# Kernel optimization log

Hardware: AMD Instinct MI355X
Metric: run time of the kernel (lower is better)

Reference implementation:

```python
import jax, jax.numpy as jnp
import numpy as np

B, S, DIN = 4, 2048, 1024
H, D = 16, 64  # num_head, per-head dim_out


def _xavier(key, shape):
    fan_in, fan_out = shape[0], shape[1]
    limit = float(np.sqrt(6.0 / (fan_in + fan_out)))
    return jax.random.uniform(key, shape, jnp.float32, -limit, limit)


def setup_inputs() -> dict:
    key = jax.random.key(0)
    k_x, k_q, k_k, k_v, k_o = jax.random.split(key, 5)
    inputs = jax.random.normal(k_x, (B, S, DIN), jnp.float32)
    # weights stored as [in, out] (transpose of torch Linear.weight); bias zeros
    return {
        "inputs": inputs,
        "wq": _xavier(k_q, (DIN, H * D)), "bq": jnp.zeros((H * D,), jnp.float32),
        "wk": _xavier(k_k, (DIN, H * D)), "bk": jnp.zeros((H * D,), jnp.float32),
        "wv": _xavier(k_v, (DIN, H * D)), "bv": jnp.zeros((H * D,), jnp.float32),
        "wo": _xavier(k_o, (H * D, D)),  "bo": jnp.zeros((D,), jnp.float32),
    }


def reference(inputs, wq, bq, wk, bk, wv, bv, wo, bo):
    b, s, _ = inputs.shape
    q = (inputs @ wq + bq).reshape(b, s, H, D).transpose(0, 2, 1, 3)  # bhsd
    k = (inputs @ wk + bk).reshape(b, s, H, D).transpose(0, 2, 1, 3)
    v = (inputs @ wv + bv).reshape(b, s, H, D).transpose(0, 2, 1, 3)
    scores = jnp.einsum('bhsd,bhSd->bhsS', q, k) / jnp.sqrt(jnp.float32(D))
    p = jax.nn.softmax(scores, axis=-1)
    o = jnp.einsum('bhsS,bhSd->bhsd', p, v)
    o = o.transpose(0, 2, 1, 3).reshape(b, s, H * D)
    return o @ wo + bo  # [b, s, D]
```

## Files before the change

kernel.cpp:

```cpp
#include <hip/hip_runtime.h>

typedef __attribute__((ext_vector_type(8))) __bf16 bf16x8;
typedef __attribute__((ext_vector_type(4))) float f32x4;

#define NB   4
#define NS   2048
#define NDIN 1024
#define NH   16
#define ND   64
#define NHD  1024
#define NM   (NB * NS)

__device__ __forceinline__ float bf2f(unsigned short u) {
    unsigned int x = ((unsigned int)u) << 16;
    return __builtin_bit_cast(float, x);
}
__device__ __forceinline__ unsigned short f2bf(float f) {
    unsigned int u = __builtin_bit_cast(unsigned int, f);
    u += 0x7fff + ((u >> 16) & 1);
    return (unsigned short)(u >> 16);
}
__device__ __forceinline__ unsigned int cvt_pk_bf16(float lo, float hi) {
    unsigned int r;
    asm("v_cvt_pk_bf16_f32 %0, %1, %2" : "=v"(r) : "v"(lo), "v"(hi));
    return r;
}
__device__ __forceinline__ void gload16(const unsigned short* g, unsigned short* l) {
    __builtin_amdgcn_global_load_lds((const __attribute__((address_space(1))) unsigned int*)g,
                                     (__attribute__((address_space(3))) unsigned int*)l, 16, 0, 0);
}

__global__ __launch_bounds__(256) void cvt_x(const float* __restrict__ src,
                                             unsigned short* __restrict__ dst) {
    int i = blockIdx.x * 256 + threadIdx.x;
    float4 a = ((const float4*)src)[i * 2];
    float4 b = ((const float4*)src)[i * 2 + 1];
    union { uint4 u; unsigned short s[8]; } o;
    o.s[0] = f2bf(a.x); o.s[1] = f2bf(a.y); o.s[2] = f2bf(a.z); o.s[3] = f2bf(a.w);
    o.s[4] = f2bf(b.x); o.s[5] = f2bf(b.y); o.s[6] = f2bf(b.z); o.s[7] = f2bf(b.w);
    *(uint4*)(dst + (size_t)i * 8) = o.u;
}

__global__ void transpose_cvt3(const float* __restrict__ wq, const float* __restrict__ wk,
                               const float* __restrict__ wv, unsigned short* __restrict__ dst_all) {
    __shared__ unsigned short t[32][33];
    const float* src = blockIdx.z == 0 ? wq : blockIdx.z == 1 ? wk : wv;
    unsigned short* dst = dst_all + (size_t)blockIdx.z * 1024 * 1024;
    int k0 = blockIdx.x * 32, n0 = blockIdx.y * 32;
    int tx = threadIdx.x, ty = threadIdx.y;
#pragma unroll
    for (int i = 0; i < 32; i += 8)
        t[ty + i][tx] = f2bf(src[(size_t)(k0 + ty + i) * 1024 + (n0 + tx)]);
    __syncthreads();
#pragma unroll
    for (int i = 0; i < 32; i += 8)
        dst[(size_t)(n0 + ty + i) * 1024 + (k0 + tx)] = t[tx][ty + i];
}

__global__ void transpose_cvt(const float* __restrict__ src,
                              unsigned short* __restrict__ dst, int K, int N) {
    __shared__ unsigned short t[32][33];
    int k0 = blockIdx.x * 32, n0 = blockIdx.y * 32;
    int tx = threadIdx.x, ty = threadIdx.y;
#pragma unroll
    for (int i = 0; i < 32; i += 8)
        t[ty + i][tx] = f2bf(src[(size_t)(k0 + ty + i) * N + (n0 + tx)]);
    __syncthreads();
#pragma unroll
    for (int i = 0; i < 32; i += 8)
        dst[(size_t)(n0 + ty + i) * K + (k0 + tx)] = t[tx][ty + i];
}

__global__ __launch_bounds__(256) void gemm_qkv(
    const unsigned short* __restrict__ X, const unsigned short* __restrict__ Wt,
    const float* __restrict__ bq, const float* __restrict__ bk,
    const float* __restrict__ bv,
    unsigned short* __restrict__ Q, unsigned short* __restrict__ K,
    unsigned short* __restrict__ V) {
    __shared__ unsigned short Al[128][32];
    __shared__ unsigned short Bl[128][32];
    __shared__ unsigned short Cl[128][128];
    int mb = blockIdx.x * 128;
    int nb = blockIdx.y * 128;
    int tid = threadIdx.x;
    int wid = tid >> 6, lane = tid & 63, quad = lane >> 4, l16 = lane & 15;
    int wm = (wid & 1) * 64, wn = (wid >> 1) * 64;

    int srow = 16 * wid + (lane >> 2);
    int scol = (lane & 3) * 8;
    const unsigned short* pa0 = X + (size_t)(mb + srow) * NDIN + scol;
    const unsigned short* pa1 = pa0 + (size_t)64 * NDIN;
    const unsigned short* pb0 = Wt + (size_t)(nb + srow) * NDIN + scol;
    const unsigned short* pb1 = pb0 + (size_t)64 * NDIN;
    unsigned short* la = &Al[0][0] + wid * 512;
    unsigned short* lb = &Bl[0][0] + wid * 512;

    f32x4 acc[4][4];
#pragma unroll
    for (int i = 0; i < 4; i++)
#pragma unroll
        for (int j = 0; j < 4; j++) acc[i][j] = (f32x4){0.f, 0.f, 0.f, 0.f};

    for (int k0 = 0; k0 < NDIN; k0 += 32) {
        gload16(pa0, la);
        gload16(pa1, la + 2048);
        gload16(pb0, lb);
        gload16(pb1, lb + 2048);
        pa0 += 32; pa1 += 32; pb0 += 32; pb1 += 32;
        __syncthreads();
        bf16x8 af[4], bfr[4];
#pragma unroll
        for (int i = 0; i < 4; i++)
            af[i] = *(const bf16x8*)(&Al[wm + i * 16 + l16][quad * 8]);
#pragma unroll
        for (int j = 0; j < 4; j++)
            bfr[j] = *(const bf16x8*)(&Bl[wn + j * 16 + l16][quad * 8]);
#pragma unroll
        for (int i = 0; i < 4; i++)
#pragma unroll
            for (int j = 0; j < 4; j++)
                acc[i][j] = __builtin_amdgcn_mfma_f32_16x16x32_bf16(af[i], bfr[j], acc[i][j], 0, 0, 0);
        __syncthreads();
    }

    int wsel = nb >> 10;
    const float* bias = (wsel == 0) ? bq : (wsel == 1) ? bk : bv;
    unsigned short* dstp = (wsel == 0) ? Q : (wsel == 1) ? K : V;
#pragma unroll
    for (int i = 0; i < 4; i++)
#pragma unroll
        for (int j = 0; j < 4; j++) {
            int nl = wn + j * 16 + l16;
            float bias_v = bias[(nb & 1023) + nl];
#pragma unroll
            for (int r = 0; r < 4; r++) {
                int ml = wm + i * 16 + quad * 4 + r;
                int pc = ((nl >> 3) ^ (ml & 15));
                Cl[ml][(pc << 3) | (nl & 7)] = f2bf(acc[i][j][r] + bias_v);
            }
        }
    __syncthreads();
    {
        int hl = tid >> 7, sl = tid & 127;
        int h = ((nb & 1023) >> 6) + hl;
        int m = mb + sl, b = m >> 11, sidx = m & 2047;
        unsigned short* orow = dstp + ((size_t)((b * NH + h) * NS + sidx)) * ND;
#pragma unroll
        for (int c = 0; c < 8; c++) {
            int pc = ((hl * 8 + c) ^ (sl & 15));
            *(uint4*)(orow + c * 8) = *(const uint4*)(&Cl[sl][pc << 3]);
        }
    }
}

__global__ __launch_bounds__(256) void attn(
    const unsigned short* __restrict__ Q, const unsigned short* __restrict__ K,
    const unsigned short* __restrict__ V, unsigned short* __restrict__ Obuf) {
    __shared__ unsigned short Kl[2][64][64];
    __shared__ unsigned short Vt[2][64][64];

    int lin = blockIdx.x;
    int xcd = lin & 7, idx = lin >> 3;
    int bh = ((idx >> 4) << 3) | xcd;
    int qt = idx & 15;

    size_t base = (size_t)bh * NS * ND;
    int tid = threadIdx.x, wid = tid >> 6, lane = tid & 63;
    int quad = lane >> 4, l16 = lane & 15;
    int lx = l16 & 7;
    int q0 = qt * 128 + wid * 32;

    bf16x8 qa[2][2];
#pragma unroll
    for (int s = 0; s < 2; s++)
#pragma unroll
        for (int f = 0; f < 2; f++) {
            union { uint4 u; unsigned short sv[8]; } in_, out_;
            in_.u = *(const uint4*)(Q + base + (size_t)(q0 + s * 16 + l16) * ND + f * 32 + quad * 8);
#pragma unroll
            for (int j = 0; j < 8; j++) out_.sv[j] = f2bf(bf2f(in_.sv[j]) * 0.125f);
            qa[s][f] = __builtin_bit_cast(bf16x8, out_.u);
        }

    float lrow[2] = {0.f, 0.f};
    f32x4 o[2][4];
#pragma unroll
    for (int s = 0; s < 2; s++)
#pragma unroll
        for (int t = 0; t < 4; t++) o[s][t] = (f32x4){0.f, 0.f, 0.f, 0.f};

    int c0 = tid, c1 = tid + 256;
    int kr0w = c0 >> 3, kc0 = c0 & 7, kg0c = kc0 ^ (kr0w & 7);
    int kr1w = c1 >> 3, kc1 = c1 & 7, kg1c = kc1 ^ (kr1w & 7);
    const unsigned short* kp0 = K + base + (size_t)kr0w * ND + kc0 * 8;
    const unsigned short* kp1 = K + base + (size_t)kr1w * ND + kc1 * 8;
    int p = tid & 31, dqA = tid >> 5, dqB = dqA + 8;
    int cp = ((p >> 4) << 2) | ((p >> 1) & 3);
    int ps = (((p >> 3) & 1) << 2) | ((p & 1) << 1);
    int cb = cp ^ ((dqA & 1) << 2);
    const unsigned short* vg = V + base + (size_t)(2 * p) * ND + dqA * 4;

    uint4 k0r, k1r;
    uint2 va0, va1, va2, va3;

    auto writeKV = [&](int buf) {
        *(uint4*)(&Kl[buf][kr0w][kg0c * 8]) = k0r;
        *(uint4*)(&Kl[buf][kr1w][kg1c * 8]) = k1r;
        unsigned short* vt = &Vt[buf][0][0];
        unsigned int w0 = __builtin_amdgcn_perm(va1.x, va0.x, 0x05040100u);
        unsigned int w1 = __builtin_amdgcn_perm(va1.x, va0.x, 0x07060302u);
        unsigned int w2 = __builtin_amdgcn_perm(va1.y, va0.y, 0x05040100u);
        unsigned int w3 = __builtin_amdgcn_perm(va1.y, va0.y, 0x07060302u);
        *(unsigned int*)(vt + (dqA * 4 + 0) * 64 + ((cb ^ 0) << 3) + ps) = w0;
        *(unsigned int*)(vt + (dqA * 4 + 1) * 64 + ((cb ^ 1) << 3) + ps) = w1;
        *(unsigned int*)(vt + (dqA * 4 + 2) * 64 + ((cb ^ 2) << 3) + ps) = w2;
        *(unsigned int*)(vt + (dqA * 4 + 3) * 64 + ((cb ^ 3) << 3) + ps) = w3;
        unsigned int x0 = __builtin_amdgcn_perm(va3.x, va2.x, 0x05040100u);
        unsigned int x1 = __builtin_amdgcn_perm(va3.x, va2.x, 0x07060302u);
        unsigned int x2 = __builtin_amdgcn_perm(va3.y, va2.y, 0x05040100u);
        unsigned int x3 = __builtin_amdgcn_perm(va3.y, va2.y, 0x07060302u);
        *(unsigned int*)(vt + (dqB * 4 + 0) * 64 + ((cb ^ 0) << 3) + ps) = x0;
        *(unsigned int*)(vt + (dqB * 4 + 1) * 64 + ((cb ^ 1) << 3) + ps) = x1;
        *(unsigned int*)(vt + (dqB * 4 + 2) * 64 + ((cb ^ 2) << 3) + ps) = x2;
        *(unsigned int*)(vt + (dqB * 4 + 3) * 64 + ((cb ^ 3) << 3) + ps) = x3;
    };

    k0r = *(const uint4*)kp0;
    k1r = *(const uint4*)kp1;
    va0 = *(const uint2*)(vg);
    va1 = *(const uint2*)(vg + ND);
    va2 = *(const uint2*)(vg + 32);
    va3 = *(const uint2*)(vg + ND + 32);
    writeKV(0);
    __syncthreads();

    int cur = 0;
    for (int kc = 0; kc < NS; kc += 64) {
        bool more = (kc + 64 < NS);
        if (more) {
            kp0 += 64 * ND; kp1 += 64 * ND; vg += 64 * ND;
            k0r = *(const uint4*)kp0;
            k1r = *(const uint4*)kp1;
            va0 = *(const uint2*)(vg);
            va1 = *(const uint2*)(vg + ND);
            va2 = *(const uint2*)(vg + 32);
            va3 = *(const uint2*)(vg + ND + 32);
        }

        const unsigned short (*Kc)[64] = Kl[cur];
        const unsigned short (*Vc)[64] = Vt[cur];

        f32x4 st[2][4];
        __builtin_amdgcn_s_setprio(1);
#pragma unroll
        for (int sub = 0; sub < 4; sub++) {
            bf16x8 kb0 = *(const bf16x8*)(&Kc[sub * 16 + l16][((quad ^ lx) << 3)]);
            bf16x8 kb1 = *(const bf16x8*)(&Kc[sub * 16 + l16][(((4 + quad) ^ lx) << 3)]);
#pragma unroll
            for (int s = 0; s < 2; s++) {
                f32x4 c = (f32x4){0.f, 0.f, 0.f, 0.f};
                c = __builtin_amdgcn_mfma_f32_16x16x32_bf16(kb0, qa[s][0], c, 0, 0, 0);
                c = __builtin_amdgcn_mfma_f32_16x16x32_bf16(kb1, qa[s][1], c, 0, 0, 0);
                st[s][sub] = c;
            }
        }
        __builtin_amdgcn_s_setprio(0);

        bf16x8 vb[4][2];
#pragma unroll
        for (int t = 0; t < 4; t++) {
            vb[t][0] = *(const bf16x8*)(&Vc[t * 16 + l16][((quad ^ lx) << 3)]);
            vb[t][1] = *(const bf16x8*)(&Vc[t * 16 + l16][(((4 + quad) ^ lx) << 3)]);
        }

        bf16x8 pb[2][2];
#pragma unroll
        for (int s = 0; s < 2; s++) {
            float sum = 0.f;
#pragma unroll
            for (int sub = 0; sub < 4; sub++)
#pragma unroll
                for (int r = 0; r < 4; r++) {
                    float pv = __expf(st[s][sub][r]);
                    st[s][sub][r] = pv;
                    sum += pv;
                }
            lrow[s] += sum;
            unsigned int a0 = cvt_pk_bf16(st[s][0][0], st[s][0][1]);
            unsigned int a1 = cvt_pk_bf16(st[s][0][2], st[s][0][3]);
            unsigned int a2 = cvt_pk_bf16(st[s][1][0], st[s][1][1]);
            unsigned int a3 = cvt_pk_bf16(st[s][1][2], st[s][1][3]);
            pb[s][0] = __builtin_bit_cast(bf16x8, (uint4){a0, a1, a2, a3});
            unsigned int b0 = cvt_pk_bf16(st[s][2][0], st[s][2][1]);
            unsigned int b1 = cvt_pk_bf16(st[s][2][2], st[s][2][3]);
            unsigned int b2 = cvt_pk_bf16(st[s][3][0], st[s][3][1]);
            unsigned int b3 = cvt_pk_bf16(st[s][3][2], st[s][3][3]);
            pb[s][1] = __builtin_bit_cast(bf16x8, (uint4){b0, b1, b2, b3});
        }

        __builtin_amdgcn_s_setprio(1);
#pragma unroll
        for (int t = 0; t < 4; t++)
#pragma unroll
            for (int s = 0; s < 2; s++) {
                o[s][t] = __builtin_amdgcn_mfma_f32_16x16x32_bf16(vb[t][0], pb[s][0], o[s][t], 0, 0, 0);
                o[s][t] = __builtin_amdgcn_mfma_f32_16x16x32_bf16(vb[t][1], pb[s][1], o[s][t], 0, 0, 0);
            }
        __builtin_amdgcn_s_setprio(0);

        if (more) {
            int nxt = cur ^ 1;
            writeKV(nxt);
            __syncthreads();
            cur = nxt;
        }
    }

    int b = bh >> 4, h = bh & 15;
#pragma unroll
    for (int s = 0; s < 2; s++) {
        float ls = lrow[s];
        ls += __shfl_xor(ls, 16, 64);
        ls += __shfl_xor(ls, 32, 64);
        float inv = 1.0f / ls;
        int q = q0 + s * 16 + l16;
#pragma unroll
        for (int t = 0; t < 4; t++) {
            uint2 w;
            w.x = cvt_pk_bf16(o[s][t][0] * inv, o[s][t][1] * inv);
            w.y = cvt_pk_bf16(o[s][t][2] * inv, o[s][t][3] * inv);
            *(uint2*)(Obuf + (size_t)(b * NS + q) * NHD + h * ND + t * 16 + quad * 4) = w;
        }
    }
}

__global__ __launch_bounds__(64) void out_proj(
    const unsigned short* __restrict__ Obuf, const unsigned short* __restrict__ WoT,
    const float* __restrict__ bo, float* __restrict__ Out) {
    int m0 = blockIdx.x * 16;
    int lane = threadIdx.x, quad = lane >> 4, l16 = lane & 15;
    f32x4 acc[4];
#pragma unroll
    for (int t = 0; t < 4; t++) acc[t] = (f32x4){0.f, 0.f, 0.f, 0.f};
    for (int k0 = 0; k0 < NHD; k0 += 32) {
        bf16x8 a = *(const bf16x8*)(Obuf + (size_t)(m0 + l16) * NHD + k0 + quad * 8);
#pragma unroll
        for (int t = 0; t < 4; t++) {
            bf16x8 b = *(const bf16x8*)(WoT + (size_t)(t * 16 + l16) * NHD + k0 + quad * 8);
            acc[t] = __builtin_amdgcn_mfma_f32_16x16x32_bf16(a, b, acc[t], 0, 0, 0);
        }
    }
#pragma unroll
    for (int t = 0; t < 4; t++) {
        int n = t * 16 + l16;
        float bb = bo[n];
#pragma unroll
        for (int r = 0; r < 4; r++) {
            int m = m0 + quad * 4 + r;
            Out[(size_t)m * ND + n] = acc[t][r] + bb;
        }
    }
}

extern "C" void kernel_launch(void* const* d_in, const int* in_sizes, int n_in,
                              void* d_out, int out_size, void* d_ws, size_t ws_size,
                              hipStream_t stream) {
    const float* X  = (const float*)d_in[0];
    const float* wq = (const float*)d_in[1];
    const float* bq = (const float*)d_in[2];
    const float* wk = (const float*)d_in[3];
    const float* bk = (const float*)d_in[4];
    const float* wv = (const float*)d_in[5];
    const float* bv = (const float*)d_in[6];
    const float* wo = (const float*)d_in[7];
    const float* bo = (const float*)d_in[8];
    float* Out = (float*)d_out;

    char* w = (char*)d_ws;
    unsigned short* Wt  = (unsigned short*)w; w += (size_t)3072 * 1024 * 2;
    unsigned short* WoT = (unsigned short*)w; w += (size_t)64 * 1024 * 2;
    unsigned short* Xb  = (unsigned short*)w; w += (size_t)NM * NDIN * 2;
    unsigned short* Qb  = (unsigned short*)w; w += (size_t)NM * NHD * 2;
    unsigned short* Kb  = (unsigned short*)w; w += (size_t)NM * NHD * 2;
    unsigned short* Vb  = (unsigned short*)w; w += (size_t)NM * NHD * 2;
    unsigned short* Ob  = (unsigned short*)w; w += (size_t)NM * NHD * 2;

    cvt_x<<<NM * NDIN / (256 * 8), 256, 0, stream>>>(X, Xb);

    dim3 tb(32, 8);
    transpose_cvt3<<<dim3(32, 32, 3), tb, 0, stream>>>(wq, wk, wv, Wt);
    transpose_cvt<<<dim3(32, 2), tb, 0, stream>>>(wo, WoT, 1024, 64);

    gemm_qkv<<<dim3(64, 24), 256, 0, stream>>>(Xb, Wt, bq, bk, bv, Qb, Kb, Vb);
    attn<<<1024, 256, 0, stream>>>(Qb, Kb, Vb, Ob);
    out_proj<<<512, 64, 0, stream>>>(Ob, WoT, bo, Out);
}
```

Measured before the change: 269.9 us.

## Alias GEMM LDS, remap tiles per XCD, split-K out_proj, defer V loads

The QKV GEMM now aliases its A/B staging buffers with the C output buffer in one shared array, cutting LDS use so more blocks can be resident. It also uses a 1D grid with an XCD-aware tile mapping so neighbouring M tiles on the same XCD share L2 data. The attention kernel loads V fragments inside the PV MFMA loop to lower register pressure. out_proj splits K across four waves per block and reduces the partial sums through LDS, giving four times the wave parallelism at the cost of a sync and an LDS reduction.

```diff
diff --git a/kernel.cpp b/kernel.cpp
--- a/kernel.cpp
+++ b/kernel.cpp
@@ -77,11 +77,17 @@
     const float* __restrict__ bv,
     unsigned short* __restrict__ Q, unsigned short* __restrict__ K,
     unsigned short* __restrict__ V) {
-    __shared__ unsigned short Al[128][32];
-    __shared__ unsigned short Bl[128][32];
-    __shared__ unsigned short Cl[128][128];
-    int mb = blockIdx.x * 128;
-    int nb = blockIdx.y * 128;
+    __shared__ unsigned short smem[128 * 128];
+    unsigned short (*Al)[32] = (unsigned short (*)[32])smem;
+    unsigned short (*Bl)[32] = (unsigned short (*)[32])(smem + 128 * 32);
+    unsigned short (*Cl)[128] = (unsigned short (*)[128])smem;
+
+    int lin = blockIdx.x;
+    int xcd = lin & 7, ii = lin >> 3;
+    int mt = xcd * 8 + (ii & 7);
+    int nt = ii >> 3;
+    int mb = mt * 128, nb = nt * 128;
+
     int tid = threadIdx.x;
     int wid = tid >> 6, lane = tid & 63, quad = lane >> 4, l16 = lane & 15;
     int wm = (wid & 1) * 64, wn = (wid >> 1) * 64;
@@ -92,8 +98,8 @@
     const unsigned short* pa1 = pa0 + (size_t)64 * NDIN;
     const unsigned short* pb0 = Wt + (size_t)(nb + srow) * NDIN + scol;
     const unsigned short* pb1 = pb0 + (size_t)64 * NDIN;
-    unsigned short* la = &Al[0][0] + wid * 512;
-    unsigned short* lb = &Bl[0][0] + wid * 512;
+    unsigned short* la = smem + wid * 512;
+    unsigned short* lb = smem + 128 * 32 + wid * 512;
 
     f32x4 acc[4][4];
 #pragma unroll
@@ -266,13 +272,6 @@
         }
         __builtin_amdgcn_s_setprio(0);
 
-        bf16x8 vb[4][2];
-#pragma unroll
-        for (int t = 0; t < 4; t++) {
-            vb[t][0] = *(const bf16x8*)(&Vc[t * 16 + l16][((quad ^ lx) << 3)]);
-            vb[t][1] = *(const bf16x8*)(&Vc[t * 16 + l16][(((4 + quad) ^ lx) << 3)]);
-        }
-
         bf16x8 pb[2][2];
 #pragma unroll
         for (int s = 0; s < 2; s++) {
@@ -300,12 +299,15 @@
 
         __builtin_amdgcn_s_setprio(1);
 #pragma unroll
-        for (int t = 0; t < 4; t++)
+        for (int t = 0; t < 4; t++) {
+            bf16x8 vb0 = *(const bf16x8*)(&Vc[t * 16 + l16][((quad ^ lx) << 3)]);
+            bf16x8 vb1 = *(const bf16x8*)(&Vc[t * 16 + l16][(((4 + quad) ^ lx) << 3)]);
 #pragma unroll
             for (int s = 0; s < 2; s++) {
-                o[s][t] = __builtin_amdgcn_mfma_f32_16x16x32_bf16(vb[t][0], pb[s][0], o[s][t], 0, 0, 0);
-                o[s][t] = __builtin_amdgcn_mfma_f32_16x16x32_bf16(vb[t][1], pb[s][1], o[s][t], 0, 0, 0);
+                o[s][t] = __builtin_amdgcn_mfma_f32_16x16x32_bf16(vb0, pb[s][0], o[s][t], 0, 0, 0);
+                o[s][t] = __builtin_amdgcn_mfma_f32_16x16x32_bf16(vb1, pb[s][1], o[s][t], 0, 0, 0);
             }
+        }
         __builtin_amdgcn_s_setprio(0);
 
         if (more) {
@@ -334,15 +336,18 @@
     }
 }
 
-__global__ __launch_bounds__(64) void out_proj(
+__global__ __launch_bounds__(256) void out_proj(
     const unsigned short* __restrict__ Obuf, const unsigned short* __restrict__ WoT,
     const float* __restrict__ bo, float* __restrict__ Out) {
+    __shared__ float red[4][16][64];
     int m0 = blockIdx.x * 16;
-    int lane = threadIdx.x, quad = lane >> 4, l16 = lane & 15;
+    int tid = threadIdx.x, wid = tid >> 6, lane = tid & 63;
+    int quad = lane >> 4, l16 = lane & 15;
     f32x4 acc[4];
 #pragma unroll
     for (int t = 0; t < 4; t++) acc[t] = (f32x4){0.f, 0.f, 0.f, 0.f};
-    for (int k0 = 0; k0 < NHD; k0 += 32) {
+    int kb = wid * 256;
+    for (int k0 = kb; k0 < kb + 256; k0 += 32) {
         bf16x8 a = *(const bf16x8*)(Obuf + (size_t)(m0 + l16) * NHD + k0 + quad * 8);
 #pragma unroll
         for (int t = 0; t < 4; t++) {
@@ -351,13 +356,23 @@
         }
     }
 #pragma unroll
-    for (int t = 0; t < 4; t++) {
-        int n = t * 16 + l16;
-        float bb = bo[n];
-#pragma unroll
-        for (int r = 0; r < 4; r++) {
-            int m = m0 + quad * 4 + r;
-            Out[(size_t)m * ND + n] = acc[t][r] + bb;
+    for (int t = 0; t < 4; t++)
+#pragma unroll
+        for (int r = 0; r < 4; r++) red[wid][t * 4 + r][lane] = acc[t][r];
+    __syncthreads();
+    if (tid < 64) {
+        int q2 = tid >> 4, s16 = tid & 15;
+#pragma unroll
+        for (int t = 0; t < 4; t++) {
+            int n = t * 16 + s16;
+            float bb = bo[n];
+#pragma unroll
+            for (int r = 0; r < 4; r++) {
+                int idx = t * 4 + r;
+                float v = red[0][idx][tid] + red[1][idx][tid] + red[2][idx][tid] + red[3][idx][tid];
+                int m = m0 + q2 * 4 + r;
+                Out[(size_t)m * ND + n] = v + bb;
+            }
         }
     }
 }
@@ -391,7 +406,7 @@
     transpose_cvt3<<<dim3(32, 32, 3), tb, 0, stream>>>(wq, wk, wv, Wt);
     transpose_cvt<<<dim3(32, 2), tb, 0, stream>>>(wo, WoT, 1024, 64);
 
-    gemm_qkv<<<dim3(64, 24), 256, 0, stream>>>(Xb, Wt, bq, bk, bv, Qb, Kb, Vb);
+    gemm_qkv<<<1536, 256, 0, stream>>>(Xb, Wt, bq, bk, bv, Qb, Kb, Vb);
     attn<<<1024, 256, 0, stream>>>(Qb, Kb, Vb, Ob);
-    out_proj<<<512, 64, 0, stream>>>(Ob, WoT, bo, Out);
-}
+    out_proj<<<512, 256, 0, stream>>>(Ob, WoT, bo, Out);
+}
```

New measurement: 277.4 us. +2.8%, slower.
